# Optimization experiments

Hardware: AMD Instinct MI355X
Metric: run time of the kernel (lower is better)

Reference implementation:

```python
import jax, jax.numpy as jnp
import numpy as np

N = 100000
E = 3200000
D = 128
EPS = 1e-12  # F.normalize default eps


def setup_inputs() -> dict:
    key = jax.random.key(0)
    ks = jax.random.split(key, 8)
    inp = {
        "edge_index": jax.random.randint(ks[0], (2, E), 0, N, dtype=jnp.int64)
        if jax.config.jax_enable_x64 else jax.random.randint(ks[0], (2, E), 0, N, dtype=jnp.int32),
        "emb_weight": jax.random.normal(ks[1], (N, D), dtype=jnp.float32) / np.sqrt(D),
        "lin_l_w0": jax.random.normal(ks[2], (D, D), dtype=jnp.float32) / np.sqrt(D),
        "lin_l_b0": jax.random.normal(ks[3], (D,), dtype=jnp.float32) * 0.01,
        "lin_r_w0": jax.random.normal(ks[4], (D, D), dtype=jnp.float32) / np.sqrt(D),
        "lin_l_w1": jax.random.normal(ks[5], (D, D), dtype=jnp.float32) / np.sqrt(D),
        "lin_l_b1": jax.random.normal(ks[6], (D,), dtype=jnp.float32) * 0.01,
        "lin_r_w1": jax.random.normal(ks[7], (D, D), dtype=jnp.float32) / np.sqrt(D),
    }
    return inp


def _sage_conv(x, src, dst, deg_inv, lin_l_w, lin_l_b, lin_r_w):
    # mean aggregation of source features at destination nodes
    agg = jax.ops.segment_sum(x[src], dst, num_segments=N) * deg_inv  # [N, D]
    # out = lin_l(agg) + lin_r(x); torch Linear: y = x @ W.T + b
    return agg @ lin_l_w.T + lin_l_b + x @ lin_r_w.T


def reference(edge_index, emb_weight, lin_l_w0, lin_l_b0, lin_r_w0,
              lin_l_w1, lin_l_b1, lin_r_w1):
    src, dst = edge_index[0], edge_index[1]
    deg = jax.ops.segment_sum(jnp.ones((E,), jnp.float32), dst, num_segments=N)
    deg_inv = jnp.where(deg > 0, 1.0 / jnp.maximum(deg, 1.0), 0.0)[:, None]  # [N,1]

    x = emb_weight
    x = _sage_conv(x, src, dst, deg_inv, lin_l_w0, lin_l_b0, lin_r_w0)
    x = jax.nn.relu(x)
    x = _sage_conv(x, src, dst, deg_inv, lin_l_w1, lin_l_b1, lin_r_w1)
    # F.normalize(x, p=2, dim=1): x / max(||x||_2, eps)
    norm = jnp.linalg.norm(x, axis=1, keepdims=True)
    return x / jnp.maximum(norm, EPS)
```

## Files before the change

### kernel.cpp

```cpp
#include <hip/hip_runtime.h>

typedef unsigned int uint;
typedef unsigned short ushort;
typedef __bf16 v8b __attribute__((ext_vector_type(8)));
typedef float v4f __attribute__((ext_vector_type(4)));

#define NN 100000
#define EE 3200000
#define DD 128

#define BSH 8
#define BSZ 256
#define NB ((NN + BSZ - 1) / BSZ)
#define CAP 16384
#define EPB 8192
#define NBLK1 ((EE + EPB - 1) / EPB)

#define LWAVES ((NN + 31) / 32)
#define LGRID ((LWAVES + 3) / 4)

__device__ __attribute__((aligned(256))) int g_offs[NN + 1];
__device__ __attribute__((aligned(256))) int g_flag[2];
__device__ __attribute__((aligned(256))) int g_bcnt2[NB];
__device__ __attribute__((aligned(256))) int g_bbase[NB];
__device__ __attribute__((aligned(256))) int g_csr[EE];
__device__ __attribute__((aligned(256))) uint g_pairs2[(size_t)NB * CAP];
__device__ __attribute__((aligned(256))) ushort g_emb_h[(size_t)NN * DD];
__device__ __attribute__((aligned(256))) ushort g_emb_l[(size_t)NN * DD];
__device__ __attribute__((aligned(256))) ushort g_agg_h[(size_t)NN * DD];
__device__ __attribute__((aligned(256))) ushort g_agg_l[(size_t)NN * DD];
__device__ __attribute__((aligned(256))) ushort g_hh[(size_t)NN * DD];
__device__ __attribute__((aligned(256))) ushort g_hl[(size_t)NN * DD];
__device__ __attribute__((aligned(256))) ushort g_w_h[4][DD * DD];
__device__ __attribute__((aligned(256))) ushort g_w_l[4][DD * DD];
__device__ __attribute__((aligned(256))) float g_biasf[2][DD];

__device__ __forceinline__ float blo(uint u) { return __uint_as_float(u << 16); }
__device__ __forceinline__ float bhi(uint u) { return __uint_as_float(u & 0xffff0000u); }
__device__ __forceinline__ ushort f2b(float f) {
  uint u = __float_as_uint(f);
  u += 0x7fffu + ((u >> 16) & 1u);
  return (ushort)(u >> 16);
}
__device__ __forceinline__ float b2f(ushort s) { return __uint_as_float(((uint)s) << 16); }

__global__ void k_detect_ei(const int* __restrict__ ei) {
  __shared__ int any;
  if (threadIdx.x == 0) any = 0;
  __syncthreads();
  int v = 0;
  for (int i = threadIdx.x; i < 2048; i += 256) v |= ei[2 * i + 1];
  if (v) atomicOr(&any, 1);
  __syncthreads();
  if (threadIdx.x == 0) g_flag[0] = (any == 0) ? 1 : 0;
}

__global__ void k_detect_f(const ushort* __restrict__ u) {
  __shared__ int bad;
  if (threadIdx.x == 0) bad = 0;
  __syncthreads();
  int b = 0;
  for (int i = threadIdx.x; i < 2048; i += 256) {
    int e = (u[2 * i] >> 7) & 0xff;
    if (e < 0x40 || e > 0x7f) b = 1;
  }
  if (b) atomicOr(&bad, 1);
  __syncthreads();
  if (threadIdx.x == 0) g_flag[1] = bad;
}

__global__ void k_split(const void* __restrict__ src, ushort* __restrict__ dh,
                        ushort* __restrict__ dl, int n) {
  int i = (blockIdx.x * blockDim.x + threadIdx.x) * 4;
  if (i >= n) return;
  float f[4];
  if (g_flag[1]) {
    float4 v = *(const float4*)((const float*)src + i);
    f[0] = v.x; f[1] = v.y; f[2] = v.z; f[3] = v.w;
  } else {
    ushort4 s = *(const ushort4*)((const ushort*)src + i);
    f[0] = b2f(s.x); f[1] = b2f(s.y); f[2] = b2f(s.z); f[3] = b2f(s.w);
  }
  ushort4 h, l;
  ushort* hp = &h.x;
  ushort* lp = &l.x;
#pragma unroll
  for (int k = 0; k < 4; k++) {
    ushort hi = f2b(f[k]);
    hp[k] = hi;
    lp[k] = f2b(f[k] - b2f(hi));
  }
  *(ushort4*)(dh + i) = h;
  *(ushort4*)(dl + i) = l;
}

__global__ void k_cvtb(const void* __restrict__ src, float* __restrict__ dst, int n) {
  int i = blockIdx.x * blockDim.x + threadIdx.x;
  if (i >= n) return;
  dst[i] = g_flag[1] ? ((const float*)src)[i] : b2f(((const ushort*)src)[i]);
}

__device__ __forceinline__ int ld_src(const int* __restrict__ ei, int is64, int e) {
  int v = is64 ? ei[2 * e] : ei[e];
  return ((uint)v < (uint)NN) ? v : 0;
}
__device__ __forceinline__ int ld_dst(const int* __restrict__ ei, int is64, int e) {
  int v = is64 ? ei[2 * (EE + e)] : ei[EE + e];
  return ((uint)v < (uint)NN) ? v : 0;
}


__global__ void k_zero2() {
  int i = threadIdx.x;
  if (i < NB) g_bcnt2[i] = 0;
}

__global__ __launch_bounds__(256) void k_bucket(const int* __restrict__ ei) {
  int is64 = g_flag[0];
  __shared__ uint s_pk[EPB];
  __shared__ ushort s_bk[EPB];
  __shared__ int s_cnt[NB];
  __shared__ int s_base[NB];
  for (int i = threadIdx.x; i < NB; i += 256) s_cnt[i] = 0;
  __syncthreads();
  int base = blockIdx.x * EPB;
#pragma unroll
  for (int i = 0; i < EPB / 256; i++) {
    int li = i * 256 + threadIdx.x;
    int e = base + li;
    uint pk = 0;
    int b = -1;
    if (e < EE) {
      int d = ld_dst(ei, is64, e);
      int s = ld_src(ei, is64, e);
      b = d >> BSH;
      pk = ((uint)(d & (BSZ - 1)) << 17) | (uint)s;
      atomicAdd(&s_cnt[b], 1);
    }
    s_pk[li] = pk;
    s_bk[li] = (ushort)b;
  }
  __syncthreads();
  for (int i = threadIdx.x; i < NB; i += 256) {
    int c = s_cnt[i];
    s_base[i] = c ? atomicAdd(&g_bcnt2[i], c) : 0;
    s_cnt[i] = 0;
  }
  __syncthreads();
#pragma unroll
  for (int i = 0; i < EPB / 256; i++) {
    int li = i * 256 + threadIdx.x;
    int b = s_bk[li];
    if (b != 0xffff) {
      int idx = s_base[b] + atomicAdd(&s_cnt[b], 1);
      if (idx < CAP) g_pairs2[(size_t)b * CAP + idx] = s_pk[li];
    }
  }
}

__global__ void k_bscan() {
  __shared__ int sd[512];
  int t = threadIdx.x;
  int v = (t < NB) ? min(g_bcnt2[t], CAP) : 0;
  sd[t] = v;
  __syncthreads();
  for (int off = 1; off < 512; off <<= 1) {
    int x = (t >= off) ? sd[t - off] : 0;
    __syncthreads();
    sd[t] += x;
    __syncthreads();
  }
  if (t < NB) g_bbase[t] = sd[t] - v;
  if (t == 511) g_offs[NN] = sd[511];
}

__global__ __launch_bounds__(256) void k_place() {
  int b = blockIdx.x;
  int n = min(g_bcnt2[b], CAP);
  int gbase = g_bbase[b];
  const uint* pr = g_pairs2 + (size_t)b * CAP;
  __shared__ int hist[BSZ];
  __shared__ int sd[BSZ];
  __shared__ int cur[BSZ];
  int t = threadIdx.x;
  hist[t] = 0;
  __syncthreads();
  for (int e = t; e < n; e += 256) atomicAdd(&hist[pr[e] >> 17], 1);
  __syncthreads();
  int v = hist[t];
  sd[t] = v;
  __syncthreads();
  for (int off = 1; off < BSZ; off <<= 1) {
    int x = (t >= off) ? sd[t - off] : 0;
    __syncthreads();
    sd[t] += x;
    __syncthreads();
  }
  int excl = sd[t] - v;
  int node = (b << BSH) + t;
  if (node < NN) g_offs[node] = gbase + excl;
  cur[t] = excl;
  __syncthreads();
  for (int e = t; e < n; e += 256) {
    uint pk = pr[e];
    int p = atomicAdd(&cur[pk >> 17], 1);
    g_csr[gbase + p] = (int)(pk & 0x1FFFFu);
  }
}

__global__ void k_agg(const ushort* __restrict__ x) {
  int lane = threadIdx.x & 63;
  int node = (blockIdx.x * blockDim.x + threadIdx.x) >> 6;
  int beg = g_offs[node], end = g_offs[node + 1];
  int eb = lane >> 4;
  int col = (lane & 15) * 8;
  float a[8];
#pragma unroll
  for (int i = 0; i < 8; i++) a[i] = 0.f;
  for (int c = beg; c < end; c += 64) {
    int cnt = end - c;
    if (cnt > 64) cnt = 64;
    int my = g_csr[c + (lane < cnt ? lane : cnt - 1)];
    if ((uint)my >= (uint)NN) my = 0;
    int j = 0;
    for (; j + 8 <= cnt; j += 8) {
      int s0 = __shfl(my, j + eb);
      int s1 = __shfl(my, j + 4 + eb);
      uint4 r0 = *(const uint4*)(x + (size_t)s0 * DD + col);
      uint4 r1 = *(const uint4*)(x + (size_t)s1 * DD + col);
      a[0] += blo(r0.x); a[1] += bhi(r0.x);
      a[2] += blo(r0.y); a[3] += bhi(r0.y);
      a[4] += blo(r0.z); a[5] += bhi(r0.z);
      a[6] += blo(r0.w); a[7] += bhi(r0.w);
      a[0] += blo(r1.x); a[1] += bhi(r1.x);
      a[2] += blo(r1.y); a[3] += bhi(r1.y);
      a[4] += blo(r1.z); a[5] += bhi(r1.z);
      a[6] += blo(r1.w); a[7] += bhi(r1.w);
    }
    for (; j < cnt; j += 4) {
      int e = j + eb;
      int s = __shfl(my, e < cnt ? e : 0);
      float w = e < cnt ? 1.f : 0.f;
      uint4 r = *(const uint4*)(x + (size_t)s * DD + col);
      a[0] = fmaf(blo(r.x), w, a[0]); a[1] = fmaf(bhi(r.x), w, a[1]);
      a[2] = fmaf(blo(r.y), w, a[2]); a[3] = fmaf(bhi(r.y), w, a[3]);
      a[4] = fmaf(blo(r.z), w, a[4]); a[5] = fmaf(bhi(r.z), w, a[5]);
      a[6] = fmaf(blo(r.w), w, a[6]); a[7] = fmaf(bhi(r.w), w, a[7]);
    }
  }
#pragma unroll
  for (int i = 0; i < 8; i++) {
    a[i] += __shfl_xor(a[i], 16);
    a[i] += __shfl_xor(a[i], 32);
  }
  int deg = end - beg;
  float inv = deg > 0 ? 1.0f / (float)deg : 0.f;
  if (lane < 16) {
    uint4 h, l;
    uint* hp = &h.x;
    uint* lp = &l.x;
#pragma unroll
    for (int k = 0; k < 4; k++) {
      float f0 = a[2 * k] * inv, f1 = a[2 * k + 1] * inv;
      ushort h0 = f2b(f0), h1 = f2b(f1);
      ushort l0 = f2b(f0 - b2f(h0)), l1 = f2b(f1 - b2f(h1));
      hp[k] = (uint)h0 | ((uint)h1 << 16);
      lp[k] = (uint)l0 | ((uint)l1 << 16);
    }
    size_t o = (size_t)node * DD + col;
    *(uint4*)(g_agg_h + o) = h;
    *(uint4*)(g_agg_l + o) = l;
  }
}


#define MFMA16(a, b, c) __builtin_amdgcn_mfma_f32_16x16x32_bf16(a, b, c, 0, 0, 0)

template <int MODE>
__global__ __launch_bounds__(256, 3) void k_lin(
    const ushort* __restrict__ A1h, const ushort* __restrict__ A1l,
    const ushort* __restrict__ A2h, const ushort* __restrict__ A2l,
    const ushort* __restrict__ Wlh, const ushort* __restrict__ Wll,
    const ushort* __restrict__ Wrh, const ushort* __restrict__ Wrl,
    const float* __restrict__ bias, void* out0, ushort* __restrict__ outlo) {
  int lane = threadIdx.x & 63;
  int wid = threadIdx.x >> 6;
  int m = lane & 15, q = lane >> 4;
  int row0 = (blockIdx.x * 4 + wid) * 32;
  if (row0 >= NN) return;
  v4f acc[2][8];
#pragma unroll
  for (int t = 0; t < 2; t++)
#pragma unroll
    for (int nt = 0; nt < 8; nt++) acc[t][nt] = (v4f){0.f, 0.f, 0.f, 0.f};
  size_t aoff0 = (size_t)(row0 + m) * DD + q * 8;
  size_t aoff1 = aoff0 + (size_t)16 * DD;
#pragma unroll
  for (int ks = 0; ks < 4; ks++) {
    v8b a1h0 = *(const v8b*)(A1h + aoff0 + ks * 32);
    v8b a1l0 = *(const v8b*)(A1l + aoff0 + ks * 32);
    v8b a2h0 = *(const v8b*)(A2h + aoff0 + ks * 32);
    v8b a2l0 = *(const v8b*)(A2l + aoff0 + ks * 32);
    v8b a1h1 = *(const v8b*)(A1h + aoff1 + ks * 32);
    v8b a1l1 = *(const v8b*)(A1l + aoff1 + ks * 32);
    v8b a2h1 = *(const v8b*)(A2h + aoff1 + ks * 32);
    v8b a2l1 = *(const v8b*)(A2l + aoff1 + ks * 32);
#pragma unroll
    for (int nt = 0; nt < 8; nt++) {
      size_t boff = (size_t)(nt * 16 + m) * DD + q * 8 + ks * 32;
      v8b blh = *(const v8b*)(Wlh + boff);
      v8b bll = *(const v8b*)(Wll + boff);
      v8b brh = *(const v8b*)(Wrh + boff);
      v8b brl = *(const v8b*)(Wrl + boff);
      acc[0][nt] = MFMA16(a1h0, blh, acc[0][nt]);
      acc[0][nt] = MFMA16(a1h0, bll, acc[0][nt]);
      acc[0][nt] = MFMA16(a1l0, blh, acc[0][nt]);
      acc[0][nt] = MFMA16(a2h0, brh, acc[0][nt]);
      acc[0][nt] = MFMA16(a2h0, brl, acc[0][nt]);
      acc[0][nt] = MFMA16(a2l0, brh, acc[0][nt]);
      acc[1][nt] = MFMA16(a1h1, blh, acc[1][nt]);
      acc[1][nt] = MFMA16(a1h1, bll, acc[1][nt]);
      acc[1][nt] = MFMA16(a1l1, blh, acc[1][nt]);
      acc[1][nt] = MFMA16(a2h1, brh, acc[1][nt]);
      acc[1][nt] = MFMA16(a2h1, brl, acc[1][nt]);
      acc[1][nt] = MFMA16(a2l1, brh, acc[1][nt]);
    }
  }
  if (MODE == 0) {
    ushort* oh = (ushort*)out0;
#pragma unroll
    for (int t = 0; t < 2; t++) {
#pragma unroll
      for (int nt = 0; nt < 8; nt++) {
        float bv = bias[nt * 16 + m];
#pragma unroll
        for (int r = 0; r < 4; r++) {
          float v = acc[t][nt][r] + bv;
          v = v > 0.f ? v : 0.f;
          ushort hi = f2b(v);
          ushort lo = f2b(v - b2f(hi));
          size_t o = (size_t)(row0 + t * 16 + q * 4 + r) * DD + nt * 16 + m;
          oh[o] = hi;
          outlo[o] = lo;
        }
      }
    }
  } else {
    float* of = (float*)out0;
#pragma unroll
    for (int t = 0; t < 2; t++) {
#pragma unroll
      for (int r = 0; r < 4; r++) {
        float p = 0.f;
#pragma unroll
        for (int nt = 0; nt < 8; nt++) {
          float v = acc[t][nt][r] + bias[nt * 16 + m];
          acc[t][nt][r] = v;
          p += v * v;
        }
        p += __shfl_xor(p, 1);
        p += __shfl_xor(p, 2);
        p += __shfl_xor(p, 4);
        p += __shfl_xor(p, 8);
        float inv = (p > 0.f) ? 1.0f / fmaxf(sqrtf(p), 1e-12f) : 0.f;
#pragma unroll
        for (int nt = 0; nt < 8; nt++)
          of[(size_t)(row0 + t * 16 + q * 4 + r) * DD + nt * 16 + m] =
              acc[t][nt][r] * inv;
      }
    }
  }
}


extern "C" void kernel_launch(void* const* d_in, const int* in_sizes, int n_in,
                              void* d_out, int out_size, void* d_ws, size_t ws_size,
                              hipStream_t stream) {
  const int* ei = (const int*)d_in[0];
  (void)in_sizes; (void)n_in; (void)out_size; (void)d_ws; (void)ws_size;

  ushort* wh;  hipGetSymbolAddress((void**)&wh, HIP_SYMBOL(g_w_h));
  ushort* wl;  hipGetSymbolAddress((void**)&wl, HIP_SYMBOL(g_w_l));
  ushort* wl0h = wh, *wr0h = wh + DD * DD, *wl1h = wh + 2 * DD * DD, *wr1h = wh + 3 * DD * DD;
  ushort* wl0l = wl, *wr0l = wl + DD * DD, *wl1l = wl + 2 * DD * DD, *wr1l = wl + 3 * DD * DD;
  float* bf;   hipGetSymbolAddress((void**)&bf, HIP_SYMBOL(g_biasf));
  float* b0 = bf, *b1 = bf + DD;
  ushort* eh;  hipGetSymbolAddress((void**)&eh, HIP_SYMBOL(g_emb_h));
  ushort* el;  hipGetSymbolAddress((void**)&el, HIP_SYMBOL(g_emb_l));
  ushort* ah;  hipGetSymbolAddress((void**)&ah, HIP_SYMBOL(g_agg_h));
  ushort* al;  hipGetSymbolAddress((void**)&al, HIP_SYMBOL(g_agg_l));
  ushort* hh;  hipGetSymbolAddress((void**)&hh, HIP_SYMBOL(g_hh));
  ushort* hl;  hipGetSymbolAddress((void**)&hl, HIP_SYMBOL(g_hl));

  k_detect_ei<<<1, 256, 0, stream>>>(ei);
  k_detect_f<<<1, 256, 0, stream>>>((const ushort*)d_in[1]);

  k_split<<<(NN * DD / 4 + 255) / 256, 256, 0, stream>>>(d_in[1], eh, el, NN * DD);
  k_split<<<(DD * DD / 4 + 255) / 256, 256, 0, stream>>>(d_in[2], wl0h, wl0l, DD * DD);
  k_split<<<(DD * DD / 4 + 255) / 256, 256, 0, stream>>>(d_in[4], wr0h, wr0l, DD * DD);
  k_split<<<(DD * DD / 4 + 255) / 256, 256, 0, stream>>>(d_in[5], wl1h, wl1l, DD * DD);
  k_split<<<(DD * DD / 4 + 255) / 256, 256, 0, stream>>>(d_in[7], wr1h, wr1l, DD * DD);
  k_cvtb<<<1, 128, 0, stream>>>(d_in[3], b0, DD);
  k_cvtb<<<1, 128, 0, stream>>>(d_in[6], b1, DD);

  k_zero2<<<1, 512, 0, stream>>>();
  k_bucket<<<NBLK1, 256, 0, stream>>>(ei);
  k_bscan<<<1, 512, 0, stream>>>();
  k_place<<<NB, 256, 0, stream>>>();

  k_agg<<<NN / 4, 256, 0, stream>>>(eh);
  k_lin<0><<<LGRID, 256, 0, stream>>>(ah, al, eh, el, wl0h, wl0l, wr0h, wr0l, b0, hh, hl);
  k_agg<<<NN / 4, 256, 0, stream>>>(hh);
  k_lin<1><<<LGRID, 256, 0, stream>>>(ah, al, hh, hl, wl1h, wl1l, wr1h, wr1l, b1, d_out, nullptr);
}
```

Baseline: 601.0 us.

## Stage weight tiles in swizzled LDS for linear kernel; fuse prep launches

The linear kernel now loads each 32-column slice of the four hi/lo weight matrices into shared memory once per block, using an XOR swizzle, instead of every wave reading the weights straight from global memory. Out-of-range rows are clamped on load and masked on store, so all waves stay active for the block-wide barriers. The embedding/weight splits, the bias conversions and the bucket-count zeroing are merged into a single prep kernel, which removes several small launches. The cost is two extra barriers per weight stage and 32 KB of LDS per block, which may lower occupancy.

```diff
diff --git a/kernel.cpp b/kernel.cpp
--- a/kernel.cpp
+++ b/kernel.cpp
@@ -16,8 +16,13 @@
 #define EPB 8192
 #define NBLK1 ((EE + EPB - 1) / EPB)
 
-#define LWAVES ((NN + 31) / 32)
-#define LGRID ((LWAVES + 3) / 4)
+#define LGRID ((NN + 127) / 128)
+
+#define PREP_EMB 12500
+#define PREP_WB 16
+#define PREP_BIAS (PREP_EMB + 4 * PREP_WB)
+#define PREP_ZERO (PREP_BIAS + 1)
+#define PREP_GRID (PREP_ZERO + 2)
 
 __device__ __attribute__((aligned(256))) int g_offs[NN + 1];
 __device__ __attribute__((aligned(256))) int g_flag[2];
@@ -69,10 +74,9 @@
   if (threadIdx.x == 0) g_flag[1] = bad;
 }
 
-__global__ void k_split(const void* __restrict__ src, ushort* __restrict__ dh,
-                        ushort* __restrict__ dl, int n) {
-  int i = (blockIdx.x * blockDim.x + threadIdx.x) * 4;
-  if (i >= n) return;
+__device__ __forceinline__ void split4(const void* __restrict__ src,
+                                       ushort* __restrict__ dh,
+                                       ushort* __restrict__ dl, int i) {
   float f[4];
   if (g_flag[1]) {
     float4 v = *(const float4*)((const float*)src + i);
@@ -94,10 +98,31 @@
   *(ushort4*)(dl + i) = l;
 }
 
-__global__ void k_cvtb(const void* __restrict__ src, float* __restrict__ dst, int n) {
-  int i = blockIdx.x * blockDim.x + threadIdx.x;
-  if (i >= n) return;
-  dst[i] = g_flag[1] ? ((const float*)src)[i] : b2f(((const ushort*)src)[i]);
+__global__ void k_prep(const void* __restrict__ emb, const void* __restrict__ s0,
+                       const void* __restrict__ s1, const void* __restrict__ s2,
+                       const void* __restrict__ s3, const void* __restrict__ bs0,
+                       const void* __restrict__ bs1) {
+  int bid = blockIdx.x;
+  int tid = threadIdx.x;
+  if (bid < PREP_EMB) {
+    int i = (bid * 256 + tid) * 4;
+    split4(emb, g_emb_h, g_emb_l, i);
+  } else if (bid < PREP_BIAS) {
+    int wb = bid - PREP_EMB;
+    int w = wb >> 4;
+    int i = ((wb & 15) * 256 + tid) * 4;
+    const void* src = (w == 0) ? s0 : (w == 1) ? s1 : (w == 2) ? s2 : s3;
+    split4(src, &g_w_h[0][0] + w * DD * DD, &g_w_l[0][0] + w * DD * DD, i);
+  } else if (bid == PREP_BIAS) {
+    int which = tid >> 7;
+    int i = tid & 127;
+    const void* src = which ? bs1 : bs0;
+    float v = g_flag[1] ? ((const float*)src)[i] : b2f(((const ushort*)src)[i]);
+    g_biasf[which][i] = v;
+  } else {
+    int i = (bid - PREP_ZERO) * 256 + tid;
+    if (i < NB) g_bcnt2[i] = 0;
+  }
 }
 
 __device__ __forceinline__ int ld_src(const int* __restrict__ ei, int is64, int e) {
@@ -109,11 +134,6 @@
   return ((uint)v < (uint)NN) ? v : 0;
 }
 
-
-__global__ void k_zero2() {
-  int i = threadIdx.x;
-  if (i < NB) g_bcnt2[i] = 0;
-}
 
 __global__ __launch_bounds__(256) void k_bucket(const int* __restrict__ ei) {
   int is64 = g_flag[0];
@@ -283,48 +303,67 @@
     const ushort* __restrict__ Wlh, const ushort* __restrict__ Wll,
     const ushort* __restrict__ Wrh, const ushort* __restrict__ Wrl,
     const float* __restrict__ bias, void* out0, ushort* __restrict__ outlo) {
-  int lane = threadIdx.x & 63;
-  int wid = threadIdx.x >> 6;
+  __shared__ ushort smem[16384];
+  int tid = threadIdx.x;
+  int lane = tid & 63;
+  int wid = tid >> 6;
   int m = lane & 15, q = lane >> 4;
-  int row0 = (blockIdx.x * 4 + wid) * 32;
-  if (row0 >= NN) return;
+  int row0 = blockIdx.x * 128 + wid * 32;
+  int arow0 = row0 + m;      if (arow0 > NN - 1) arow0 = NN - 1;
+  int arow1 = row0 + 16 + m; if (arow1 > NN - 1) arow1 = NN - 1;
+  size_t aoff0 = (size_t)arow0 * DD + q * 8;
+  size_t aoff1 = (size_t)arow1 * DD + q * 8;
   v4f acc[2][8];
 #pragma unroll
   for (int t = 0; t < 2; t++)
 #pragma unroll
     for (int nt = 0; nt < 8; nt++) acc[t][nt] = (v4f){0.f, 0.f, 0.f, 0.f};
-  size_t aoff0 = (size_t)(row0 + m) * DD + q * 8;
-  size_t aoff1 = aoff0 + (size_t)16 * DD;
-#pragma unroll
-  for (int ks = 0; ks < 4; ks++) {
-    v8b a1h0 = *(const v8b*)(A1h + aoff0 + ks * 32);
-    v8b a1l0 = *(const v8b*)(A1l + aoff0 + ks * 32);
-    v8b a2h0 = *(const v8b*)(A2h + aoff0 + ks * 32);
-    v8b a2l0 = *(const v8b*)(A2l + aoff0 + ks * 32);
-    v8b a1h1 = *(const v8b*)(A1h + aoff1 + ks * 32);
-    v8b a1l1 = *(const v8b*)(A1l + aoff1 + ks * 32);
-    v8b a2h1 = *(const v8b*)(A2h + aoff1 + ks * 32);
-    v8b a2l1 = *(const v8b*)(A2l + aoff1 + ks * 32);
-#pragma unroll
-    for (int nt = 0; nt < 8; nt++) {
-      size_t boff = (size_t)(nt * 16 + m) * DD + q * 8 + ks * 32;
-      v8b blh = *(const v8b*)(Wlh + boff);
-      v8b bll = *(const v8b*)(Wll + boff);
-      v8b brh = *(const v8b*)(Wrh + boff);
-      v8b brl = *(const v8b*)(Wrl + boff);
-      acc[0][nt] = MFMA16(a1h0, blh, acc[0][nt]);
-      acc[0][nt] = MFMA16(a1h0, bll, acc[0][nt]);
-      acc[0][nt] = MFMA16(a1l0, blh, acc[0][nt]);
-      acc[0][nt] = MFMA16(a2h0, brh, acc[0][nt]);
-      acc[0][nt] = MFMA16(a2h0, brl, acc[0][nt]);
-      acc[0][nt] = MFMA16(a2l0, brh, acc[0][nt]);
-      acc[1][nt] = MFMA16(a1h1, blh, acc[1][nt]);
-      acc[1][nt] = MFMA16(a1h1, bll, acc[1][nt]);
-      acc[1][nt] = MFMA16(a1l1, blh, acc[1][nt]);
-      acc[1][nt] = MFMA16(a2h1, brh, acc[1][nt]);
-      acc[1][nt] = MFMA16(a2h1, brl, acc[1][nt]);
-      acc[1][nt] = MFMA16(a2l1, brh, acc[1][nt]);
-    }
+#pragma unroll
+  for (int st = 0; st < 4; st++) {
+#pragma unroll
+    for (int k = 0; k < 8; k++) {
+      int arr = k >> 1;
+      int n = ((k & 1) << 4) + (tid >> 4);
+      int cb16 = tid & 15;
+      const ushort* srcp = (arr == 0) ? Wlh : (arr == 1) ? Wll : (arr == 2) ? Wrh : Wrl;
+      uint4 v = *(const uint4*)(srcp + (size_t)(st * 32 + n) * DD + cb16 * 8);
+      *(uint4*)(smem + arr * 4096 + n * 128 + ((cb16 ^ (n & 15)) << 3)) = v;
+    }
+    __syncthreads();
+#pragma unroll
+    for (int ks = 0; ks < 4; ks++) {
+      v8b a1h0 = *(const v8b*)(A1h + aoff0 + ks * 32);
+      v8b a1l0 = *(const v8b*)(A1l + aoff0 + ks * 32);
+      v8b a2h0 = *(const v8b*)(A2h + aoff0 + ks * 32);
+      v8b a2l0 = *(const v8b*)(A2l + aoff0 + ks * 32);
+      v8b a1h1 = *(const v8b*)(A1h + aoff1 + ks * 32);
+      v8b a1l1 = *(const v8b*)(A1l + aoff1 + ks * 32);
+      v8b a2h1 = *(const v8b*)(A2h + aoff1 + ks * 32);
+      v8b a2l1 = *(const v8b*)(A2l + aoff1 + ks * 32);
+#pragma unroll
+      for (int ntl = 0; ntl < 2; ntl++) {
+        int nt = st * 2 + ntl;
+        int nl = ntl * 16 + m;
+        int u = nl * 128 + (((q + 4 * ks) ^ m) << 3);
+        v8b blh = *(const v8b*)(smem + u);
+        v8b bll = *(const v8b*)(smem + 4096 + u);
+        v8b brh = *(const v8b*)(smem + 8192 + u);
+        v8b brl = *(const v8b*)(smem + 12288 + u);
+        acc[0][nt] = MFMA16(a1h0, blh, acc[0][nt]);
+        acc[0][nt] = MFMA16(a1h0, bll, acc[0][nt]);
+        acc[0][nt] = MFMA16(a1l0, blh, acc[0][nt]);
+        acc[0][nt] = MFMA16(a2h0, brh, acc[0][nt]);
+        acc[0][nt] = MFMA16(a2h0, brl, acc[0][nt]);
+        acc[0][nt] = MFMA16(a2l0, brh, acc[0][nt]);
+        acc[1][nt] = MFMA16(a1h1, blh, acc[1][nt]);
+        acc[1][nt] = MFMA16(a1h1, bll, acc[1][nt]);
+        acc[1][nt] = MFMA16(a1l1, blh, acc[1][nt]);
+        acc[1][nt] = MFMA16(a2h1, brh, acc[1][nt]);
+        acc[1][nt] = MFMA16(a2h1, brl, acc[1][nt]);
+        acc[1][nt] = MFMA16(a2l1, brh, acc[1][nt]);
+      }
+    }
+    __syncthreads();
   }
   if (MODE == 0) {
     ushort* oh = (ushort*)out0;
@@ -335,13 +374,16 @@
         float bv = bias[nt * 16 + m];
 #pragma unroll
         for (int r = 0; r < 4; r++) {
-          float v = acc[t][nt][r] + bv;
-          v = v > 0.f ? v : 0.f;
-          ushort hi = f2b(v);
-          ushort lo = f2b(v - b2f(hi));
-          size_t o = (size_t)(row0 + t * 16 + q * 4 + r) * DD + nt * 16 + m;
-          oh[o] = hi;
-          outlo[o] = lo;
+          int row = row0 + t * 16 + q * 4 + r;
+          if (row < NN) {
+            float v = acc[t][nt][r] + bv;
+            v = v > 0.f ? v : 0.f;
+            ushort hi = f2b(v);
+            ushort lo = f2b(v - b2f(hi));
+            size_t o = (size_t)row * DD + nt * 16 + m;
+            oh[o] = hi;
+            outlo[o] = lo;
+          }
         }
       }
     }
@@ -363,10 +405,12 @@
         p += __shfl_xor(p, 4);
         p += __shfl_xor(p, 8);
         float inv = (p > 0.f) ? 1.0f / fmaxf(sqrtf(p), 1e-12f) : 0.f;
-#pragma unroll
-        for (int nt = 0; nt < 8; nt++)
-          of[(size_t)(row0 + t * 16 + q * 4 + r) * DD + nt * 16 + m] =
-              acc[t][nt][r] * inv;
+        int row = row0 + t * 16 + q * 4 + r;
+        if (row < NN) {
+#pragma unroll
+          for (int nt = 0; nt < 8; nt++)
+            of[(size_t)row * DD + nt * 16 + m] = acc[t][nt][r] * inv;
+        }
       }
     }
   }
@@ -395,15 +439,9 @@
   k_detect_ei<<<1, 256, 0, stream>>>(ei);
   k_detect_f<<<1, 256, 0, stream>>>((const ushort*)d_in[1]);
 
-  k_split<<<(NN * DD / 4 + 255) / 256, 256, 0, stream>>>(d_in[1], eh, el, NN * DD);
-  k_split<<<(DD * DD / 4 + 255) / 256, 256, 0, stream>>>(d_in[2], wl0h, wl0l, DD * DD);
-  k_split<<<(DD * DD / 4 + 255) / 256, 256, 0, stream>>>(d_in[4], wr0h, wr0l, DD * DD);
-  k_split<<<(DD * DD / 4 + 255) / 256, 256, 0, stream>>>(d_in[5], wl1h, wl1l, DD * DD);
-  k_split<<<(DD * DD / 4 + 255) / 256, 256, 0, stream>>>(d_in[7], wr1h, wr1l, DD * DD);
-  k_cvtb<<<1, 128, 0, stream>>>(d_in[3], b0, DD);
-  k_cvtb<<<1, 128, 0, stream>>>(d_in[6], b1, DD);
-
-  k_zero2<<<1, 512, 0, stream>>>();
+  k_prep<<<PREP_GRID, 256, 0, stream>>>(d_in[1], d_in[2], d_in[4], d_in[5],
+                                        d_in[7], d_in[3], d_in[6]);
+
   k_bucket<<<NBLK1, 256, 0, stream>>>(ei);
   k_bscan<<<1, 512, 0, stream>>>();
   k_place<<<NB, 256, 0, stream>>>();
```

Measured after the change: 673.9 us. +12.1%, slower.
